# Kernel optimization log

Measured on AMD Instinct MI355X. Metric: run time of the kernel, lower is better.

Reference implementation:

```python
import jax, jax.numpy as jnp
import numpy as np

HIDDEN = 1024
NUM_HEAD = 16
HEAD_DIM = HIDDEN // NUM_HEAD


def setup_inputs() -> dict:
    key = jax.random.key(0)
    ks = jax.random.split(key, 9)
    B, S = 1, 4096
    scale = 1.0 / np.sqrt(HIDDEN)
    inp = {
        "x": jax.random.normal(ks[0], (B, S, HIDDEN), dtype=jnp.float32),
        "wq": jax.random.normal(ks[1], (HIDDEN, HIDDEN), dtype=jnp.float32) * scale,
        "bq": jnp.zeros((HIDDEN,), dtype=jnp.float32),
        "wk": jax.random.normal(ks[2], (HIDDEN, HIDDEN), dtype=jnp.float32) * scale,
        "bk": jnp.zeros((HIDDEN,), dtype=jnp.float32),
        "wv": jax.random.normal(ks[3], (HIDDEN, HIDDEN), dtype=jnp.float32) * scale,
        "bv": jnp.zeros((HIDDEN,), dtype=jnp.float32),
        "wo": jax.random.normal(ks[4], (HIDDEN, HIDDEN), dtype=jnp.float32) * scale,
        "bo": jnp.zeros((HIDDEN,), dtype=jnp.float32),
    }
    return inp


def reference(x, wq, bq, wk, bk, wv, bv, wo, bo):
    B, S, _ = x.shape
    # QKV projections (torch Linear: x @ W.T + b)
    def split_heads(t):
        return t.reshape(B, S, NUM_HEAD, HEAD_DIM).transpose(0, 2, 1, 3)  # [B,H,S,D]
    q = split_heads(x @ wq.T + bq)
    k = split_heads(x @ wk.T + bk)
    v = split_heads(x @ wv.T + bv)
    # scaled dot-product scores: [B,H,S,S]
    scores = jnp.einsum('bhsd,bhtd->bhst', q, k) / jnp.sqrt(jnp.float32(HEAD_DIM))
    # faithful double softmax over the key axis (no mask; dropout = eval identity)
    attn = jax.nn.softmax(scores, axis=-1)
    attn = jax.nn.softmax(attn, axis=-1)
    out = jnp.einsum('bhst,bhtd->bhsd', attn, v)  # [B,H,S,D]
    out = out.transpose(0, 2, 1, 3).reshape(B, S, HIDDEN)
    return out @ wo.T + bo
```

## Files before the change

kernel.cpp:

```cpp
#include <hip/hip_runtime.h>
#include <hip/hip_bf16.h>
#include <stdint.h>

#define S 4096
#define HID 1024
#define NH 16
#define DH 64

typedef __attribute__((ext_vector_type(8))) short short8;
typedef __attribute__((ext_vector_type(2))) float f32x2;
typedef __attribute__((ext_vector_type(4))) float f32x4;
typedef __attribute__((ext_vector_type(16))) float f32x16;
typedef __attribute__((ext_vector_type(4))) unsigned int u32x4;

#define VMCNT8 asm volatile("s_waitcnt vmcnt(8)" ::: "memory")
#define VMCNT0 asm volatile("s_waitcnt vmcnt(0)" ::: "memory")
#define LGKM0  asm volatile("s_waitcnt lgkmcnt(0)" ::: "memory")

__device__ __forceinline__ unsigned short f2bf(float f) {
  unsigned int u = __builtin_bit_cast(unsigned int, f);
  u += 0x7FFF + ((u >> 16) & 1);
  return (unsigned short)(u >> 16);
}
__device__ __forceinline__ unsigned int pktrunc(float lo, float hi) {
  return __builtin_amdgcn_perm(__builtin_bit_cast(unsigned int, hi),
                               __builtin_bit_cast(unsigned int, lo), 0x07060302u);
}
__device__ __forceinline__ void gload16(const unsigned short* g, unsigned short* l) {
  __builtin_amdgcn_global_load_lds((const __attribute__((address_space(1))) unsigned int*)g,
                                   (__attribute__((address_space(3))) unsigned int*)l, 16, 0, 0);
}

__global__ __launch_bounds__(256) void cast_kernel(
    const float* __restrict__ x,  const float* __restrict__ wq,
    const float* __restrict__ wk, const float* __restrict__ wv,
    const float* __restrict__ wo,
    unsigned short* __restrict__ xb,  unsigned short* __restrict__ wqb,
    unsigned short* __restrict__ wkb, unsigned short* __restrict__ wvb,
    unsigned short* __restrict__ wob)
{
  int y = blockIdx.y;
  const float* src; unsigned short* dst; int n;
  if      (y == 0) { src = x;  dst = xb;  n = S * HID; }
  else if (y == 1) { src = wq; dst = wqb; n = HID * HID; }
  else if (y == 2) { src = wk; dst = wkb; n = HID * HID; }
  else if (y == 3) { src = wv; dst = wvb; n = HID * HID; }
  else             { src = wo; dst = wob; n = HID * HID; }
  int i = (blockIdx.x * 256 + threadIdx.x) * 4;
  if (i < n) {
    float4 v = *reinterpret_cast<const float4*>(src + i);
    ushort4 o;
    o.x = f2bf(v.x); o.y = f2bf(v.y); o.z = f2bf(v.z); o.w = f2bf(v.w);
    *reinterpret_cast<ushort4*>(dst + i) = o;
  }
}

__device__ __forceinline__ void gemm128(
    const unsigned short* __restrict__ A, const unsigned short* __restrict__ W,
    unsigned short* As, unsigned short* Bs, f32x4 acc[4][4], int row0, int col0)
{
  const int tid = threadIdx.x;
  const int wave = tid >> 6, lane = tid & 63, quad = lane >> 4, l16 = lane & 15;
  const int wr = (wave >> 1) * 64, wc = (wave & 1) * 64;
  const int srow = lane >> 2, sseg = lane & 3;
  const f32x4 z = {0.f, 0.f, 0.f, 0.f};
  #pragma unroll
  for (int i = 0; i < 4; i++)
    #pragma unroll
    for (int j = 0; j < 4; j++) acc[i][j] = z;

  for (int k0 = 0; k0 < HID; k0 += 32) {
    __syncthreads();
    #pragma unroll
    for (int c = 0; c < 2; c++) {
      const int rbase = c * 64 + wave * 16;
      gload16(A + (size_t)(row0 + rbase + srow) * HID + k0 + sseg * 8, As + rbase * 32);
      gload16(W + (size_t)(col0 + rbase + srow) * HID + k0 + sseg * 8, Bs + rbase * 32);
    }
    __syncthreads();

    short8 af[4], bfr[4];
    #pragma unroll
    for (int i = 0; i < 4; i++)
      af[i] = *reinterpret_cast<const short8*>(As + (wr + i * 16 + l16) * 32 + quad * 8);
    #pragma unroll
    for (int j = 0; j < 4; j++)
      bfr[j] = *reinterpret_cast<const short8*>(Bs + (wc + j * 16 + l16) * 32 + quad * 8);
    #pragma unroll
    for (int i = 0; i < 4; i++)
      #pragma unroll
      for (int j = 0; j < 4; j++)
        acc[i][j] = __builtin_amdgcn_mfma_f32_16x16x32_bf16(af[i], bfr[j], acc[i][j], 0, 0, 0);
  }
}

__global__ __launch_bounds__(256) void qkv_gemm_kernel(
    const unsigned short* __restrict__ X,
    const unsigned short* __restrict__ Wq, const unsigned short* __restrict__ Wk,
    const unsigned short* __restrict__ Wv,
    const float* __restrict__ bq, const float* __restrict__ bk, const float* __restrict__ bv,
    unsigned short* __restrict__ Qo, unsigned short* __restrict__ K2o, unsigned short* __restrict__ Vbo,
    float* __restrict__ Vsum)
{
  __shared__ unsigned short As[128 * 32];
  __shared__ unsigned short Bs[128 * 32];
  const int zsel = blockIdx.z;
  const unsigned short* W = (zsel == 0) ? Wq : (zsel == 1) ? Wk : Wv;
  const float* bias        = (zsel == 0) ? bq : (zsel == 1) ? bk : bv;
  const int row0 = blockIdx.x * 128, col0 = blockIdx.y * 128;
  f32x4 acc[4][4];
  gemm128(X, W, As, Bs, acc, row0, col0);

  const int tid = threadIdx.x;
  const int wave = tid >> 6, lane = tid & 63, quad = lane >> 4, l16 = lane & 15;
  const int wr = (wave >> 1) * 64, wc = (wave & 1) * 64;

  if (zsel == 0) {
    const float osc = 0.18033688011112042f;
    #pragma unroll
    for (int j = 0; j < 4; j++) {
      int n = col0 + wc + j * 16 + l16;
      float bb = bias[n];
      int h = n >> 6, d = n & 63;
      #pragma unroll
      for (int i = 0; i < 4; i++)
        #pragma unroll
        for (int rr = 0; rr < 4; rr++) {
          int s = row0 + wr + i * 16 + quad * 4 + rr;
          Qo[(size_t)(h * S + s) * DH + d] = f2bf((acc[i][j][rr] + bb) * osc);
        }
    }
  } else if (zsel == 1) {
    #pragma unroll
    for (int j = 0; j < 4; j++) {
      int n = col0 + wc + j * 16 + l16;
      float bb = bias[n];
      int h = n >> 6, dh = n & 63;
      int c = dh >> 4, hfk = (dh >> 3) & 1, j8 = dh & 7;
      #pragma unroll
      for (int i = 0; i < 4; i++)
        #pragma unroll
        for (int rr = 0; rr < 4; rr++) {
          int s = row0 + wr + i * 16 + quad * 4 + rr;
          int g = s >> 5, l32k = s & 31;
          K2o[((size_t)((h * 128 + g) * 4 + c) * 64 + hfk * 32 + l32k) * 8 + j8] =
              f2bf(acc[i][j][rr] + bb);
        }
    }
  } else {
    #pragma unroll
    for (int j = 0; j < 4; j++) {
      int n = col0 + wc + j * 16 + l16;
      float bb = bias[n];
      int h = n >> 6, dh = n & 63;
      int ng = dh >> 5, l32v = dh & 31;
      int hf_v = quad & 1, jj0 = (quad >> 1) * 4;
      float colsum = 0.f;
      #pragma unroll
      for (int i = 0; i < 4; i++) {
        int gt = (row0 + wr + i * 16) >> 5;
        int grp = i & 1;
        float v0 = acc[i][j][0] + bb, v1 = acc[i][j][1] + bb;
        float v2 = acc[i][j][2] + bb, v3 = acc[i][j][3] + bb;
        colsum += (v0 + v1) + (v2 + v3);
        ushort4 pv;
        pv.x = f2bf(v0); pv.y = f2bf(v1); pv.z = f2bf(v2); pv.w = f2bf(v3);
        *reinterpret_cast<ushort4*>(
            Vbo + ((size_t)(((h * 128 + gt) * 2 + grp) * 2 + ng) * 64 + hf_v * 32 + l32v) * 8 + jj0) = pv;
      }
      colsum += __shfl_xor(colsum, 16);
      colsum += __shfl_xor(colsum, 32);
      if (quad == 0) atomicAdd(&Vsum[n], colsum);
    }
  }
}

__global__ __launch_bounds__(256) void out_gemm_kernel(
    const unsigned short* __restrict__ A, const unsigned short* __restrict__ W,
    const float* __restrict__ be, float* __restrict__ dst)
{
  __shared__ unsigned short As[128 * 32];
  __shared__ unsigned short Bs[128 * 32];
  const int row0 = blockIdx.x * 128, col0 = blockIdx.y * 128;
  f32x4 acc[4][4];
  gemm128(A, W, As, Bs, acc, row0, col0);

  const int tid = threadIdx.x;
  const int wave = tid >> 6, lane = tid & 63, quad = lane >> 4, l16 = lane & 15;
  const int wr = (wave >> 1) * 64, wc = (wave & 1) * 64;
  #pragma unroll
  for (int j = 0; j < 4; j++) {
    int n = col0 + wc + j * 16 + l16;
    float bb = be[n];
    #pragma unroll
    for (int i = 0; i < 4; i++)
      #pragma unroll
      for (int rr = 0; rr < 4; rr++) {
        int s = row0 + wr + i * 16 + quad * 4 + rr;
        dst[(size_t)s * HID + n] = acc[i][j][rr] + bb;
      }
  }
}

__global__ __launch_bounds__(256) void biasfold_kernel(
    const float* __restrict__ Vsum, const float* __restrict__ wo,
    const float* __restrict__ bo, float* __restrict__ be)
{
  const int n = blockIdx.x * 4 + (threadIdx.x >> 6);
  const int l = threadIdx.x & 63;
  float acc = 0.f;
  #pragma unroll
  for (int i = 0; i < 16; i++)
    acc += Vsum[l + 64 * i] * wo[(size_t)n * HID + l + 64 * i];
  #pragma unroll
  for (int off = 32; off >= 1; off >>= 1) acc += __shfl_xor(acc, off);
  if (l == 0) be[n] = bo[n] + acc * (1.f / 4097.f);
}

struct AttnState {
  short8 qf[2][4];
  f32x16 Oa[2][2];
  f32x16 zacc;
  f32x2  zp[2];
};

__device__ __forceinline__ void loadregs(
    const unsigned short* kb, const unsigned short* vb,
    short8 (&kf)[4], short8 (&vf)[4])
{
  #pragma unroll
  for (int c = 0; c < 4; c++)
    kf[c] = *reinterpret_cast<const short8*>(kb + c * 512);
  #pragma unroll
  for (int w = 0; w < 4; w++)
    vf[w] = *reinterpret_cast<const short8*>(vb + w * 512);
}

__device__ __forceinline__ void attn_compute(
    const short8 (&kf)[4], const short8 (&vfr)[4], AttnState& st)
{
  #pragma unroll
  for (int qh = 0; qh < 2; qh++) {
    f32x16 acc = __builtin_amdgcn_mfma_f32_32x32x16_bf16(kf[0], st.qf[qh][0], st.zacc, 0, 0, 0);
    #pragma unroll
    for (int c = 1; c < 4; c++)
      acc = __builtin_amdgcn_mfma_f32_32x32x16_bf16(kf[c], st.qf[qh][c], acc, 0, 0, 0);

    unsigned int D[8];
    #pragma unroll
    for (int m = 0; m < 8; m++) {
      float t0 = __builtin_amdgcn_exp2f(acc[2 * m]);
      float t1 = __builtin_amdgcn_exp2f(acc[2 * m + 1]);
      f32x2 t = {t0, t1};
      st.zp[qh] += t;
      D[m] = pktrunc(t0, t1);
    }
    u32x4 dv0 = {D[0], D[1], D[2], D[3]};
    u32x4 dv1 = {D[4], D[5], D[6], D[7]};
    short8 A0 = __builtin_bit_cast(short8, dv0);
    short8 A1 = __builtin_bit_cast(short8, dv1);

    st.Oa[qh][0] = __builtin_amdgcn_mfma_f32_32x32x16_bf16(A0, vfr[0], st.Oa[qh][0], 0, 0, 0);
    st.Oa[qh][1] = __builtin_amdgcn_mfma_f32_32x32x16_bf16(A0, vfr[1], st.Oa[qh][1], 0, 0, 0);
    st.Oa[qh][0] = __builtin_amdgcn_mfma_f32_32x32x16_bf16(A1, vfr[2], st.Oa[qh][0], 0, 0, 0);
    st.Oa[qh][1] = __builtin_amdgcn_mfma_f32_32x32x16_bf16(A1, vfr[3], st.Oa[qh][1], 0, 0, 0);
  }
}

__device__ __forceinline__ void stage_tile(
    const unsigned short* gK, const unsigned short* gV,
    unsigned short* lK, unsigned short* lV)
{
  #pragma unroll
  for (int i = 0; i < 4; i++) gload16(gK + i * 512, lK + i * 512);
  #pragma unroll
  for (int i = 0; i < 4; i++) gload16(gV + i * 512, lV + i * 512);
}

__global__ __launch_bounds__(256, 2) void attn_kernel(
    const unsigned short* __restrict__ Q, const unsigned short* __restrict__ K2,
    const unsigned short* __restrict__ Vb, unsigned short* __restrict__ OUT)
{
  __shared__ unsigned short T[4][2][2][2048];
  __shared__ float Zl[256];
  float* Ored = reinterpret_cast<float*>(&T[0][0][0][0]);

  const int lin = blockIdx.y * 64 + blockIdx.x;
  const int xcd = lin & 7, idx = lin >> 3;
  const int h = xcd * 2 + (idx >> 6);
  const int q0 = (idx & 63) * 64;

  const int tid = threadIdx.x;
  const int wave = tid >> 6, lane = tid & 63, hf = lane >> 5, l32 = lane & 31;

  AttnState st;
  #pragma unroll
  for (int qh = 0; qh < 2; qh++) {
    const unsigned short* qrow = Q + (size_t)(h * S + q0 + qh * 32 + l32) * DH;
    #pragma unroll
    for (int c = 0; c < 4; c++)
      st.qf[qh][c] = *reinterpret_cast<const short8*>(qrow + c * 16 + hf * 8);
  }
  #pragma unroll
  for (int r = 0; r < 16; r++) {
    st.zacc[r] = 0.f;
    st.Oa[0][0][r] = 0.f; st.Oa[0][1][r] = 0.f;
    st.Oa[1][0][r] = 0.f; st.Oa[1][1][r] = 0.f;
  }
  st.zp[0] = (f32x2){0.f, 0.f};
  st.zp[1] = (f32x2){0.f, 0.f};

  const unsigned short* Kb  = K2 + (size_t)h * 128 * 2048;
  const unsigned short* Vbb = Vb + (size_t)h * 128 * 2048;

  const unsigned short* gK = Kb  + (size_t)wave * 2048 + (size_t)lane * 8;
  const unsigned short* gV = Vbb + (size_t)wave * 2048 + (size_t)lane * 8;
  unsigned short* lK0 = &T[wave][0][0][0];
  unsigned short* lV0 = &T[wave][0][1][0];
  unsigned short* lK1 = &T[wave][1][0][0];
  unsigned short* lV1 = &T[wave][1][1][0];
  const unsigned short* kb0 = &T[wave][0][0][0] + lane * 8;
  const unsigned short* vb0 = &T[wave][0][1][0] + lane * 8;
  const unsigned short* kb1 = &T[wave][1][0][0] + lane * 8;
  const unsigned short* vb1 = &T[wave][1][1][0] + lane * 8;
  const ptrdiff_t STR = 4 * 2048;

  short8 kA[4], vA[4], kB[4], vB[4];

  stage_tile(gK, gV, lK0, lV0); gK += STR; gV += STR;
  VMCNT0;
  loadregs(kb0, vb0, kA, vA);
  stage_tile(gK, gV, lK1, lV1); gK += STR; gV += STR;
  LGKM0;

  for (int p = 0; p < 15; p++) {
    stage_tile(gK, gV, lK0, lV0); gK += STR; gV += STR;
    VMCNT8;
    loadregs(kb1, vb1, kB, vB);
    attn_compute(kA, vA, st);
    LGKM0;
    stage_tile(gK, gV, lK1, lV1); gK += STR; gV += STR;
    VMCNT8;
    loadregs(kb0, vb0, kA, vA);
    attn_compute(kB, vB, st);
    LGKM0;
  }
  VMCNT0;
  loadregs(kb1, vb1, kB, vB);
  attn_compute(kA, vA, st);
  attn_compute(kB, vB, st);

  __syncthreads();
  {
    float za = st.zp[0][0] + st.zp[0][1];
    float zb = st.zp[1][0] + st.zp[1][1];
    za += __shfl_xor(za, 32);
    zb += __shfl_xor(zb, 32);
    if (hf == 0) {
      Zl[wave * 64 + l32]      = za;
      Zl[wave * 64 + 32 + l32] = zb;
    }
    float* Ow = Ored + wave * 4096;
    #pragma unroll
    for (int qh = 0; qh < 2; qh++)
      #pragma unroll
      for (int ng = 0; ng < 2; ng++)
        #pragma unroll
        for (int r = 0; r < 16; r++) {
          const int row = (r & 3) + 8 * (r >> 2) + 4 * hf;
          Ow[(qh * 32 + row) * 64 + ng * 32 + l32] = st.Oa[qh][ng][r];
        }
  }
  __syncthreads();
  {
    const int q = tid >> 2, d0 = (tid & 3) * 16;
    const float* O0 = Ored + q * 64 + d0;
    f32x4 s0 = *reinterpret_cast<const f32x4*>(O0);
    f32x4 s1 = *reinterpret_cast<const f32x4*>(O0 + 4);
    f32x4 s2 = *reinterpret_cast<const f32x4*>(O0 + 8);
    f32x4 s3 = *reinterpret_cast<const f32x4*>(O0 + 12);
    #pragma unroll
    for (int w = 1; w < 4; w++) {
      const float* Ow = Ored + w * 4096 + q * 64 + d0;
      s0 += *reinterpret_cast<const f32x4*>(Ow);
      s1 += *reinterpret_cast<const f32x4*>(Ow + 4);
      s2 += *reinterpret_cast<const f32x4*>(Ow + 8);
      s3 += *reinterpret_cast<const f32x4*>(Ow + 12);
    }
    const float zt = Zl[q] + Zl[64 + q] + Zl[128 + q] + Zl[192 + q];
    const float rz = 1.f / (zt * 4097.f);
    unsigned short* op = OUT + (size_t)(q0 + q) * HID + h * DH + d0;
    ushort4 u;
    u.x = f2bf(s0[0] * rz); u.y = f2bf(s0[1] * rz);
    u.z = f2bf(s0[2] * rz); u.w = f2bf(s0[3] * rz);
    *reinterpret_cast<ushort4*>(op) = u;
    u.x = f2bf(s1[0] * rz); u.y = f2bf(s1[1] * rz);
    u.z = f2bf(s1[2] * rz); u.w = f2bf(s1[3] * rz);
    *reinterpret_cast<ushort4*>(op + 4) = u;
    u.x = f2bf(s2[0] * rz); u.y = f2bf(s2[1] * rz);
    u.z = f2bf(s2[2] * rz); u.w = f2bf(s2[3] * rz);
    *reinterpret_cast<ushort4*>(op + 8) = u;
    u.x = f2bf(s3[0] * rz); u.y = f2bf(s3[1] * rz);
    u.z = f2bf(s3[2] * rz); u.w = f2bf(s3[3] * rz);
    *reinterpret_cast<ushort4*>(op + 12) = u;
  }
}

extern "C" void kernel_launch(void* const* d_in, const int* in_sizes, int n_in,
                              void* d_out, int out_size, void* d_ws, size_t ws_size,
                              hipStream_t stream) {
  const float* x  = (const float*)d_in[0];
  const float* wq = (const float*)d_in[1];
  const float* bq = (const float*)d_in[2];
  const float* wk = (const float*)d_in[3];
  const float* bk = (const float*)d_in[4];
  const float* wv = (const float*)d_in[5];
  const float* bv = (const float*)d_in[6];
  const float* wo = (const float*)d_in[7];
  const float* bo = (const float*)d_in[8];
  float* out = (float*)d_out;

  char* ws = (char*)d_ws;
  unsigned short* xb  = (unsigned short*)(ws);
  unsigned short* wqb = (unsigned short*)(ws + (8u  << 20));
  unsigned short* wkb = (unsigned short*)(ws + (10u << 20));
  unsigned short* wvb = (unsigned short*)(ws + (12u << 20));
  unsigned short* wob = (unsigned short*)(ws + (14u << 20));
  unsigned short* qw  = (unsigned short*)(ws + (16u << 20));
  unsigned short* k2  = (unsigned short*)(ws + (24u << 20));
  unsigned short* vb  = (unsigned short*)(ws + (32u << 20));
  float* vsum         = (float*)(ws + (40u << 20));
  float* be           = (float*)(ws + (40u << 20) + 65536);
  unsigned short* aw  = xb;

  hipMemsetAsync(vsum, 0, 1024 * sizeof(float), stream);
  cast_kernel<<<dim3(4096, 5), 256, 0, stream>>>(x, wq, wk, wv, wo, xb, wqb, wkb, wvb, wob);
  qkv_gemm_kernel<<<dim3(32, 8, 3), 256, 0, stream>>>(xb, wqb, wkb, wvb, bq, bk, bv, qw, k2, vb, vsum);
  biasfold_kernel<<<dim3(256), 256, 0, stream>>>(vsum, wo, bo, be);
  attn_kernel<<<dim3(64, 16), 256, 0, stream>>>(qw, k2, vb, aw);
  out_gemm_kernel<<<dim3(32, 8, 1), 256, 0, stream>>>(aw, wob, be, out);
}
```

Baseline: 238.4 us.

## Stage QKV epilogue through LDS for coalesced stores, fold vsum memset into cast

New measurement: 234.3 us. No clear change (-1.7%).

```diff
diff --git a/kernel.cpp b/kernel.cpp
--- a/kernel.cpp
+++ b/kernel.cpp
@@ -37,7 +37,7 @@
     const float* __restrict__ wo,
     unsigned short* __restrict__ xb,  unsigned short* __restrict__ wqb,
     unsigned short* __restrict__ wkb, unsigned short* __restrict__ wvb,
-    unsigned short* __restrict__ wob)
+    unsigned short* __restrict__ wob, float* __restrict__ vsum)
 {
   int y = blockIdx.y;
   const float* src; unsigned short* dst; int n;
@@ -46,6 +46,10 @@
   else if (y == 2) { src = wk; dst = wkb; n = HID * HID; }
   else if (y == 3) { src = wv; dst = wvb; n = HID * HID; }
   else             { src = wo; dst = wob; n = HID * HID; }
+  if (y == 0 && blockIdx.x == 0) {
+    f32x4 z = {0.f, 0.f, 0.f, 0.f};
+    reinterpret_cast<f32x4*>(vsum)[threadIdx.x] = z;
+  }
   int i = (blockIdx.x * 256 + threadIdx.x) * 4;
   if (i < n) {
     float4 v = *reinterpret_cast<const float4*>(src + i);
@@ -104,6 +108,7 @@
 {
   __shared__ unsigned short As[128 * 32];
   __shared__ unsigned short Bs[128 * 32];
+  __shared__ unsigned short Ep[16384];
   const int zsel = blockIdx.z;
   const unsigned short* W = (zsel == 0) ? Wq : (zsel == 1) ? Wk : Wv;
   const float* bias        = (zsel == 0) ? bq : (zsel == 1) ? bk : bv;
@@ -114,51 +119,52 @@
   const int tid = threadIdx.x;
   const int wave = tid >> 6, lane = tid & 63, quad = lane >> 4, l16 = lane & 15;
   const int wr = (wave >> 1) * 64, wc = (wave & 1) * 64;
+  const int h0 = col0 >> 6, g0 = row0 >> 5;
 
   if (zsel == 0) {
     const float osc = 0.18033688011112042f;
     #pragma unroll
     for (int j = 0; j < 4; j++) {
-      int n = col0 + wc + j * 16 + l16;
-      float bb = bias[n];
-      int h = n >> 6, d = n & 63;
+      int rc = wc + j * 16 + l16;
+      float bb = bias[col0 + rc];
+      int hh = rc >> 6, d = rc & 63;
       #pragma unroll
       for (int i = 0; i < 4; i++)
         #pragma unroll
         for (int rr = 0; rr < 4; rr++) {
-          int s = row0 + wr + i * 16 + quad * 4 + rr;
-          Qo[(size_t)(h * S + s) * DH + d] = f2bf((acc[i][j][rr] + bb) * osc);
+          int srel = wr + i * 16 + quad * 4 + rr;
+          Ep[hh * 8192 + srel * 64 + d] = f2bf((acc[i][j][rr] + bb) * osc);
         }
     }
   } else if (zsel == 1) {
     #pragma unroll
     for (int j = 0; j < 4; j++) {
-      int n = col0 + wc + j * 16 + l16;
-      float bb = bias[n];
-      int h = n >> 6, dh = n & 63;
+      int rc = wc + j * 16 + l16;
+      float bb = bias[col0 + rc];
+      int hh = rc >> 6, dh = rc & 63;
       int c = dh >> 4, hfk = (dh >> 3) & 1, j8 = dh & 7;
       #pragma unroll
       for (int i = 0; i < 4; i++)
         #pragma unroll
         for (int rr = 0; rr < 4; rr++) {
-          int s = row0 + wr + i * 16 + quad * 4 + rr;
-          int g = s >> 5, l32k = s & 31;
-          K2o[((size_t)((h * 128 + g) * 4 + c) * 64 + hfk * 32 + l32k) * 8 + j8] =
+          int srel = wr + i * 16 + quad * 4 + rr;
+          int gl = srel >> 5, l32k = srel & 31;
+          Ep[(hh * 4 + gl) * 2048 + (c * 64 + hfk * 32 + l32k) * 8 + j8] =
               f2bf(acc[i][j][rr] + bb);
         }
     }
   } else {
     #pragma unroll
     for (int j = 0; j < 4; j++) {
-      int n = col0 + wc + j * 16 + l16;
-      float bb = bias[n];
-      int h = n >> 6, dh = n & 63;
+      int rc = wc + j * 16 + l16;
+      float bb = bias[col0 + rc];
+      int hh = rc >> 6, dh = rc & 63;
       int ng = dh >> 5, l32v = dh & 31;
       int hf_v = quad & 1, jj0 = (quad >> 1) * 4;
       float colsum = 0.f;
       #pragma unroll
       for (int i = 0; i < 4; i++) {
-        int gt = (row0 + wr + i * 16) >> 5;
+        int gt4 = (wr + i * 16) >> 5;
         int grp = i & 1;
         float v0 = acc[i][j][0] + bb, v1 = acc[i][j][1] + bb;
         float v2 = acc[i][j][2] + bb, v3 = acc[i][j][3] + bb;
@@ -166,11 +172,32 @@
         ushort4 pv;
         pv.x = f2bf(v0); pv.y = f2bf(v1); pv.z = f2bf(v2); pv.w = f2bf(v3);
         *reinterpret_cast<ushort4*>(
-            Vbo + ((size_t)(((h * 128 + gt) * 2 + grp) * 2 + ng) * 64 + hf_v * 32 + l32v) * 8 + jj0) = pv;
+            Ep + (((hh * 4 + gt4) * 2 + grp) * 2 + ng) * 512 + (hf_v * 32 + l32v) * 8 + jj0) = pv;
       }
       colsum += __shfl_xor(colsum, 16);
       colsum += __shfl_xor(colsum, 32);
-      if (quad == 0) atomicAdd(&Vsum[n], colsum);
+      if (quad == 0) atomicAdd(&Vsum[col0 + rc], colsum);
+    }
+  }
+  __syncthreads();
+
+  #pragma unroll
+  for (int it = 0; it < 8; it++) {
+    int flat = it * 2048 + tid * 8;
+    u32x4 v = *reinterpret_cast<const u32x4*>(Ep + flat);
+    if (zsel == 0) {
+      int hh = flat >> 13;
+      size_t goff = ((size_t)(h0 + hh) * S + row0) * 64 + (flat & 8191);
+      *reinterpret_cast<u32x4*>(Qo + goff) = v;
+    } else if (zsel == 1) {
+      int sp = flat >> 11, hh = sp >> 2, g4 = sp & 3;
+      size_t goff = (size_t)((h0 + hh) * 128 + g0 + g4) * 2048 + (flat & 2047);
+      *reinterpret_cast<u32x4*>(K2o + goff) = v;
+    } else {
+      int sp = flat >> 9;
+      int ng = sp & 1, grp = (sp >> 1) & 1, gt4 = (sp >> 2) & 3, hh = sp >> 4;
+      size_t goff = (size_t)((((h0 + hh) * 128 + g0 + gt4) * 2 + grp) * 2 + ng) * 512 + (flat & 511);
+      *reinterpret_cast<u32x4*>(Vbo + goff) = v;
     }
   }
 }
@@ -433,8 +460,7 @@
   float* be           = (float*)(ws + (40u << 20) + 65536);
   unsigned short* aw  = xb;
 
-  hipMemsetAsync(vsum, 0, 1024 * sizeof(float), stream);
-  cast_kernel<<<dim3(4096, 5), 256, 0, stream>>>(x, wq, wk, wv, wo, xb, wqb, wkb, wvb, wob);
+  cast_kernel<<<dim3(4096, 5), 256, 0, stream>>>(x, wq, wk, wv, wo, xb, wqb, wkb, wvb, wob, vsum);
   qkv_gemm_kernel<<<dim3(32, 8, 3), 256, 0, stream>>>(xb, wqb, wkb, wvb, bq, bk, bv, qw, k2, vb, vsum);
   biasfold_kernel<<<dim3(256), 256, 0, stream>>>(vsum, wo, bo, be);
   attn_kernel<<<dim3(64, 16), 256, 0, stream>>>(qw, k2, vb, aw);
```
